# Kernel tuning notes

Hardware: AMD Instinct MI355X
Metric: run time of the kernel (lower is better)

Reference implementation:

```python
import jax, jax.numpy as jnp
import numpy as np
from jax import lax

DIM = 256          # C
D_INNER = 512      # expand * dim
D_STATE = 16       # N
DT_RANK = 32       # ceil(d_inner / 16)
K_CONV = 4


def setup_inputs() -> dict:
    key = jax.random.key(0)
    ks = jax.random.split(key, 20)
    B, C, H, W = 2, DIM, 64, 64
    Di, N, R = D_INNER, D_STATE, DT_RANK
    s = 0.02
    inp = {
        "decoder_feat": jax.random.normal(ks[0], (B, C, H, W), jnp.float32),
        "encoder_feat": jax.random.normal(ks[1], (B, C, H, W), jnp.float32),
        # CrossMambaFusion params
        "dec_w": jax.random.normal(ks[2], (C, 2 * Di), jnp.float32) * s,
        "dec_b": jnp.zeros((2 * Di,), jnp.float32),
        "enc_w": jax.random.normal(ks[3], (C, Di), jnp.float32) * s,
        "enc_b": jnp.zeros((Di,), jnp.float32),
        "out_w": jax.random.normal(ks[4], (Di, C), jnp.float32) * s,
        "out_b": jnp.zeros((C,), jnp.float32),
        "ln_g": jnp.ones((C,), jnp.float32),
        "ln_b": jnp.zeros((C,), jnp.float32),
        # Mamba block params (inner dim = Di, expand=1.0)
        "in_w": jax.random.normal(ks[5], (Di, 2 * Di), jnp.float32) * s,
        "in_b": jnp.zeros((2 * Di,), jnp.float32),
        "conv_w": jax.random.normal(ks[6], (Di, 1, K_CONV), jnp.float32) * 0.1,
        "conv_b": jnp.zeros((Di,), jnp.float32),
        "x_proj_w": jax.random.normal(ks[7], (Di, R + 2 * N), jnp.float32) * s,
        "dt_w": jax.random.normal(ks[8], (R, Di), jnp.float32) * 0.1,
        "dt_b": jax.random.uniform(ks[9], (Di,), jnp.float32, -4.0, -2.0),  # small dt after softplus
        "A_log": jnp.log(jnp.tile(jnp.arange(1, N + 1, dtype=jnp.float32)[None, :], (Di, 1))),
        "D_param": jnp.ones((Di,), jnp.float32),
        "m_out_w": jax.random.normal(ks[10], (Di, Di), jnp.float32) * s,
        "m_out_b": jnp.zeros((Di,), jnp.float32),
    }
    return inp


def _mamba(x, in_w, in_b, conv_w, conv_b, x_proj_w, dt_w, dt_b, A_log, D_param, m_out_w, m_out_b):
    # x: (B, L, Di)
    Bsz, L, Di = x.shape
    N, R = D_STATE, DT_RANK
    xz = x @ in_w + in_b                      # (B, L, 2*Di)
    xm, z = jnp.split(xz, 2, axis=-1)
    # causal depthwise conv over the sequence axis
    xc = jnp.swapaxes(xm, 1, 2)               # (B, Di, L)
    xc = lax.conv_general_dilated(
        xc, conv_w, window_strides=(1,), padding=[(K_CONV - 1, 0)],
        dimension_numbers=("NCH", "OIH", "NCH"), feature_group_count=Di)
    xc = xc + conv_b[None, :, None]
    u = jax.nn.silu(jnp.swapaxes(xc, 1, 2))   # (B, L, Di)
    x_dbl = u @ x_proj_w                      # (B, L, R+2N)
    dt = jax.nn.softplus(x_dbl[..., :R] @ dt_w + dt_b)   # (B, L, Di)
    Bm = x_dbl[..., R:R + N]                  # (B, L, N)
    Cm = x_dbl[..., R + N:]                   # (B, L, N)
    A = -jnp.exp(A_log)                       # (Di, N)

    def step(h, t):
        dt_t, u_t, B_t, C_t = t               # (B,Di),(B,Di),(B,N),(B,N)
        dA = jnp.exp(dt_t[..., None] * A)     # (B, Di, N)
        h = h * dA + (dt_t * u_t)[..., None] * B_t[:, None, :]
        y = jnp.einsum("bdn,bn->bd", h, C_t)
        return h, y

    h0 = jnp.zeros((Bsz, Di, N), x.dtype)
    _, ys = lax.scan(step, h0, (jnp.swapaxes(dt, 0, 1), jnp.swapaxes(u, 0, 1),
                                jnp.swapaxes(Bm, 0, 1), jnp.swapaxes(Cm, 0, 1)))
    y = jnp.swapaxes(ys, 0, 1) + u * D_param  # skip connection via D
    y = y * jax.nn.silu(z)
    return y @ m_out_w + m_out_b


def reference(decoder_feat, encoder_feat, dec_w, dec_b, enc_w, enc_b, out_w, out_b,
              ln_g, ln_b, in_w, in_b, conv_w, conv_b, x_proj_w, dt_w, dt_b,
              A_log, D_param, m_out_w, m_out_b):
    B, C, H, W = decoder_feat.shape
    Di = D_INNER
    dec = jnp.transpose(decoder_feat, (0, 2, 3, 1)).reshape(B, H * W, C)
    enc = jnp.transpose(encoder_feat, (0, 2, 3, 1)).reshape(B, H * W, C)
    dec_proj = dec @ dec_w + dec_b
    dec_x, dec_gate = dec_proj[..., :Di], dec_proj[..., Di:]
    enc_p = enc @ enc_w + enc_b
    combined = dec_x * jax.nn.sigmoid(enc_p) + enc_p          # (B, L, Di)
    processed = _mamba(combined, in_w, in_b, conv_w, conv_b, x_proj_w,
                       dt_w, dt_b, A_log, D_param, m_out_w, m_out_b)
    out = (processed * jax.nn.sigmoid(dec_gate)) @ out_w + out_b
    res = out + dec
    mu = jnp.mean(res, axis=-1, keepdims=True)
    var = jnp.mean(jnp.square(res - mu), axis=-1, keepdims=True)
    res = (res - mu) * lax.rsqrt(var + 1e-5) * ln_g + ln_b
    return jnp.transpose(res.reshape(B, H, W, C), (0, 3, 1, 2))
```

## Files before the change

kernel.cpp:

```cpp
#include <hip/hip_runtime.h>
#include <hip/hip_bf16.h>

typedef __bf16 bf16x8_t __attribute__((ext_vector_type(8)));
typedef float f32x4_t __attribute__((ext_vector_type(4)));

__device__ __forceinline__ float sigmoidf_(float x) { return 1.0f / (1.0f + __expf(-x)); }
__device__ __forceinline__ float siluf_(float x) { return x * sigmoidf_(x); }
__device__ __forceinline__ float softplusf_(float x) {
    return fmaxf(x, 0.0f) + log1pf(__expf(-fabsf(x)));
}
__device__ __forceinline__ float b2f(ushort u) { return __uint_as_float(((unsigned)u) << 16); }
__device__ __forceinline__ ushort f2b(float f) {
    return (ushort)__bfloat16_as_ushort(__float2bfloat16(f));
}

__global__ __launch_bounds__(256) void k_prep(
    const float* __restrict__ dec_w, const float* __restrict__ enc_w,
    const float* __restrict__ in_w, const float* __restrict__ m_out_w,
    const float* __restrict__ out_w, const float* __restrict__ x_proj_w,
    const float* __restrict__ dt_w,
    const float* __restrict__ dec, const float* __restrict__ enc,
    __hip_bfloat16* __restrict__ dec_wT, __hip_bfloat16* __restrict__ enc_wT,
    __hip_bfloat16* __restrict__ in_wT, __hip_bfloat16* __restrict__ m_out_wT,
    __hip_bfloat16* __restrict__ out_wT, __hip_bfloat16* __restrict__ xpwT,
    __hip_bfloat16* __restrict__ dtwT,
    __hip_bfloat16* __restrict__ decL, __hip_bfloat16* __restrict__ encL)
{
    __shared__ float tile[64][65];
    if (blockIdx.x < 5312) {
        int gid = blockIdx.x * 256 + threadIdx.x;
        const float* src; __hip_bfloat16* dst; int lk, N, idx;
        if (gid < 262144)       { src = dec_w;    dst = dec_wT;   lk = 8; N = 1024; idx = gid; }
        else if (gid < 393216)  { src = enc_w;    dst = enc_wT;   lk = 8; N = 512;  idx = gid - 262144; }
        else if (gid < 917504)  { src = in_w;     dst = in_wT;    lk = 9; N = 1024; idx = gid - 393216; }
        else if (gid < 1179648) { src = m_out_w;  dst = m_out_wT; lk = 9; N = 512;  idx = gid - 917504; }
        else if (gid < 1310720) { src = out_w;    dst = out_wT;   lk = 9; N = 256;  idx = gid - 1179648; }
        else if (gid < 1343488) { src = x_proj_w; dst = xpwT;     lk = 9; N = 64;   idx = gid - 1310720; }
        else                    { src = dt_w;     dst = dtwT;     lk = 5; N = 512;  idx = gid - 1343488; }
        int K = 1 << lk;
        int n = idx >> lk, k = idx & (K - 1);
        dst[idx] = __float2bfloat16(src[(size_t)k * N + n]);
        return;
    }
    const int bid = blockIdx.x - 5312;
    const int t = threadIdx.x;
    const int ct = bid & 3;
    const int lt = (bid >> 2) & 63;
    const int sel = bid >> 8;
    const int b = sel & 1, ten = sel >> 1;
    const float* src = ten ? enc : dec;
    __hip_bfloat16* dst = ten ? encL : decL;
    const size_t ibase = (size_t)b * 256 * 4096 + (size_t)(ct * 64) * 4096 + (size_t)lt * 64;
#pragma unroll
    for (int i = 0; i < 16; ++i) {
        int c = i * 4 + (t >> 6), l = t & 63;
        tile[c][l] = src[ibase + (size_t)c * 4096 + l];
    }
    __syncthreads();
    const size_t obase = ((size_t)b * 4096 + (size_t)lt * 64) * 256 + ct * 64;
#pragma unroll
    for (int i = 0; i < 16; ++i) {
        int l = i * 4 + (t >> 6), c = t & 63;
        dst[obase + (size_t)l * 256 + c] = __float2bfloat16(tile[c][l]);
    }
}

template <int EPI, int K>
__global__ __launch_bounds__(256) void bgemm(
    const __hip_bfloat16* __restrict__ A, const __hip_bfloat16* __restrict__ Bt,
    const float* __restrict__ bias, void* __restrict__ out0,
    void* __restrict__ out1, const void* __restrict__ extra)
{
    __shared__ ushort At[128 * 32];
    __shared__ ushort Bl[128 * 32];
    const int tid = threadIdx.x;
    const int wave = tid >> 6, lane = tid & 63;
    const int n0 = blockIdx.x * 128, m0 = blockIdx.y * 128;
    const int wm = (wave >> 1) * 64, wn = (wave & 1) * 64;
    f32x4_t acc[4][4] = {};
    const int fr = lane & 15, fq = (lane >> 4) * 8;

    for (int k0 = 0; k0 < K; k0 += 32) {
#pragma unroll
        for (int q = 0; q < 2; ++q) {
            int idx = q * 256 + tid;
            int row = idx >> 2, ch = (idx & 3) * 8;
            uint4 va = *(const uint4*)&A[(size_t)(m0 + row) * K + k0 + ch];
            uint4 vb = *(const uint4*)&Bt[(size_t)(n0 + row) * K + k0 + ch];
            *(uint4*)&At[row * 32 + ch] = va;
            *(uint4*)&Bl[row * 32 + ch] = vb;
        }
        __syncthreads();
        bf16x8_t af[4], bf[4];
#pragma unroll
        for (int i = 0; i < 4; ++i) {
            af[i] = *(bf16x8_t*)&At[(wm + i * 16 + fr) * 32 + fq];
            bf[i] = *(bf16x8_t*)&Bl[(wn + i * 16 + fr) * 32 + fq];
        }
#pragma unroll
        for (int i = 0; i < 4; ++i)
#pragma unroll
            for (int j = 0; j < 4; ++j)
                acc[i][j] = __builtin_amdgcn_mfma_f32_16x16x32_bf16(af[i], bf[j], acc[i][j], 0, 0, 0);
        __syncthreads();
    }

    const int col = lane & 15, rbase = (lane >> 4) * 4;
#pragma unroll
    for (int i = 0; i < 4; ++i) {
#pragma unroll
        for (int j = 0; j < 4; ++j) {
#pragma unroll
            for (int r = 0; r < 4; ++r) {
                int m = m0 + wm + i * 16 + rbase + r;
                int n = n0 + wn + j * 16 + col;
                float v = acc[i][j][r] + bias[n];
                if (EPI == 0) {
                    ((__hip_bfloat16*)out0)[(size_t)m * 512 + n] = __float2bfloat16(v);
                } else if (EPI == 1) {
                    if (n < 512) {
                        float ep = __bfloat162float(((const __hip_bfloat16*)extra)[(size_t)m * 512 + n]);
                        ((__hip_bfloat16*)out0)[(size_t)m * 512 + n] =
                            __float2bfloat16(fmaf(v, sigmoidf_(ep), ep));
                    } else {
                        ((__hip_bfloat16*)out1)[(size_t)m * 512 + (n - 512)] =
                            __float2bfloat16(sigmoidf_(v));
                    }
                } else if (EPI == 2) {
                    if (n < 512)
                        ((__hip_bfloat16*)out0)[(size_t)m * 512 + n] = __float2bfloat16(v);
                    else
                        ((__hip_bfloat16*)out1)[(size_t)m * 512 + (n - 512)] =
                            __float2bfloat16(siluf_(v));
                } else {
                    float g = __bfloat162float(((const __hip_bfloat16*)extra)[(size_t)m * 512 + n]);
                    ((__hip_bfloat16*)out0)[(size_t)m * 512 + n] = __float2bfloat16(v * g);
                }
            }
        }
    }
}

#define CHUNK 32
#define NCHUNK 128

__global__ __launch_bounds__(512) void k_conv_scan(
    const __hip_bfloat16* __restrict__ xm, const float* __restrict__ conv_w,
    const float* __restrict__ conv_b, const __hip_bfloat16* __restrict__ xpwT,
    const __hip_bfloat16* __restrict__ dtwT, const float* __restrict__ dt_b,
    const float* __restrict__ A_log,
    __hip_bfloat16* __restrict__ u_out, float* __restrict__ Bm,
    float* __restrict__ Cm, __hip_bfloat16* __restrict__ dt_out,
    float* __restrict__ hpart, float* __restrict__ dtsums)
{
    __shared__ __align__(16) ushort us_dts[CHUNK][512 + 8];
    __shared__ __align__(16) ushort adt[CHUNK][32 + 8];
    __shared__ float BsL[CHUNK * 16];
    __shared__ float CsL[CHUNK * 16];
    const int tid = threadIdx.x;
    const int wave = tid >> 6, lane = tid & 63;
    const int bl0 = blockIdx.x * CHUNK;
    const int l0 = bl0 & 4095;
    const int b = blockIdx.x >> 7;
    const int chunk = blockIdx.x & (NCHUNK - 1);
    const int fr = lane & 15, fq = (lane >> 4) * 8;
    const int col = lane & 15, rbase = (lane >> 4) * 4;

    float uarr[CHUNK];
    {
        const int d = tid;
        const float cw0 = conv_w[d * 4], cw1 = conv_w[d * 4 + 1];
        const float cw2 = conv_w[d * 4 + 2], cw3 = conv_w[d * 4 + 3];
        const float cb = conv_b[d];
        const ushort* xs = (const ushort*)xm;
        float x0 = (l0 >= 3) ? b2f(xs[(size_t)(bl0 - 3) * 512 + d]) : 0.f;
        float x1 = (l0 >= 2) ? b2f(xs[(size_t)(bl0 - 2) * 512 + d]) : 0.f;
        float x2 = (l0 >= 1) ? b2f(xs[(size_t)(bl0 - 1) * 512 + d]) : 0.f;
#pragma unroll
        for (int t = 0; t < CHUNK; ++t) {
            float x3 = b2f(xs[(size_t)(bl0 + t) * 512 + d]);
            float a = cb;
            a = fmaf(cw0, x0, a);
            a = fmaf(cw1, x1, a);
            a = fmaf(cw2, x2, a);
            a = fmaf(cw3, x3, a);
            float uv = siluf_(a);
            uarr[t] = uv;
            ushort ub = f2b(uv);
            us_dts[t][d] = ub;
            ((ushort*)u_out)[(size_t)(bl0 + t) * 512 + d] = ub;
            x0 = x1; x1 = x2; x2 = x3;
        }
    }
    __syncthreads();

    {
        const int mi = wave >> 2, n0w = (wave & 3) * 16;
        f32x4_t acc = {};
        const __hip_bfloat16* bp = xpwT + (size_t)(n0w + fr) * 512;
#pragma unroll
        for (int k0 = 0; k0 < 512; k0 += 32) {
            bf16x8_t af = *(bf16x8_t*)&us_dts[mi * 16 + fr][k0 + fq];
            bf16x8_t bf = *(const bf16x8_t*)&bp[k0 + fq];
            acc = __builtin_amdgcn_mfma_f32_16x16x32_bf16(af, bf, acc, 0, 0, 0);
        }
#pragma unroll
        for (int r = 0; r < 4; ++r) {
            int m = mi * 16 + rbase + r;
            int n = n0w + col;
            float v = acc[r];
            if (n < 32) {
                adt[m][n] = f2b(v);
            } else if (n < 48) {
                BsL[m * 16 + (n - 32)] = v;
                Bm[(size_t)(bl0 + m) * 16 + (n - 32)] = v;
            } else {
                CsL[m * 16 + (n - 48)] = v;
                Cm[(size_t)(bl0 + m) * 16 + (n - 48)] = v;
            }
        }
    }
    __syncthreads();

    {
        const int mi = wave >> 2;
        bf16x8_t af = *(bf16x8_t*)&adt[mi * 16 + fr][fq];
#pragma unroll
        for (int t = 0; t < 8; ++t) {
            int nt = (wave & 3) * 8 + t;
            bf16x8_t bf = *(const bf16x8_t*)&dtwT[(size_t)(nt * 16 + fr) * 32 + fq];
            f32x4_t acc = {};
            acc = __builtin_amdgcn_mfma_f32_16x16x32_bf16(af, bf, acc, 0, 0, 0);
#pragma unroll
            for (int r = 0; r < 4; ++r) {
                int m = mi * 16 + rbase + r;
                int n = nt * 16 + col;
                ushort dv = f2b(softplusf_(acc[r] + dt_b[n]));
                us_dts[m][n] = dv;
                ((ushort*)dt_out)[(size_t)(bl0 + m) * 512 + n] = dv;
            }
        }
    }
    __syncthreads();

    {
        const int d = tid;
        float Av[16];
#pragma unroll
        for (int n = 0; n < 16; n += 4) {
            float4 al = *(const float4*)&A_log[d * 16 + n];
            Av[n + 0] = -__expf(al.x);
            Av[n + 1] = -__expf(al.y);
            Av[n + 2] = -__expf(al.z);
            Av[n + 3] = -__expf(al.w);
        }
        float h[16] = {};
        float dtsum = 0.f;
#pragma unroll
        for (int t = 0; t < CHUNK; ++t) {
            float dtv = b2f(us_dts[t][d]);
            float dtu = dtv * uarr[t];
            dtsum += dtv;
            const float* Bt = &BsL[t * 16];
#pragma unroll
            for (int n = 0; n < 16; ++n)
                h[n] = fmaf(h[n], __expf(dtv * Av[n]), dtu * Bt[n]);
        }
        const size_t sidx = ((size_t)b * NCHUNK + chunk) * 512 + d;
        const size_t idx = sidx * 16;
#pragma unroll
        for (int n = 0; n < 16; n += 4)
            *(float4*)&hpart[idx + n] = make_float4(h[n], h[n + 1], h[n + 2], h[n + 3]);
        dtsums[sidx] = dtsum;
    }
}

__global__ __launch_bounds__(256) void k_scan_comb(
    const float* __restrict__ hpart, const float* __restrict__ dtsums,
    const float* __restrict__ A_log, float* __restrict__ h_in)
{
    const int gid = blockIdx.x * 256 + threadIdx.x;
    const int n = gid & 15;
    const int d = (gid >> 4) & 511;
    const int b = gid >> 13;
    const float Av = -__expf(A_log[d * 16 + n]);
    float h = 0.f;
    for (int c = 0; c < NCHUNK; ++c) {
        const size_t sidx = ((size_t)b * NCHUNK + c) * 512 + d;
        const size_t idx = sidx * 16 + n;
        h_in[idx] = h;
        h = fmaf(h, __expf(Av * dtsums[sidx]), hpart[idx]);
    }
}

__global__ __launch_bounds__(512) void k_scan_fin(
    const __hip_bfloat16* __restrict__ dt, const __hip_bfloat16* __restrict__ u,
    const float* __restrict__ Bmp, const float* __restrict__ Cmp,
    const float* __restrict__ A_log, const float* __restrict__ Dp,
    const __hip_bfloat16* __restrict__ zs, const float* __restrict__ h_in,
    __hip_bfloat16* __restrict__ yout)
{
    __shared__ float Bs[CHUNK * 16];
    __shared__ float Cs[CHUNK * 16];
    const int d = threadIdx.x;
    const int chunk = blockIdx.x & (NCHUNK - 1);
    const int b = blockIdx.x >> 7;
    const size_t row0 = (size_t)b * 4096 + (size_t)chunk * CHUNK;

    Bs[d] = Bmp[row0 * 16 + d];
    Cs[d] = Cmp[row0 * 16 + d];
    float Av[16];
#pragma unroll
    for (int n = 0; n < 16; n += 4) {
        float4 al = *(const float4*)&A_log[d * 16 + n];
        Av[n + 0] = -__expf(al.x);
        Av[n + 1] = -__expf(al.y);
        Av[n + 2] = -__expf(al.z);
        Av[n + 3] = -__expf(al.w);
    }
    const float Dv = Dp[d];
    float h[16];
    const size_t idx = (((size_t)b * NCHUNK + chunk) * 512 + d) * 16;
#pragma unroll
    for (int n = 0; n < 16; n += 4) {
        float4 hv = *(const float4*)&h_in[idx + n];
        h[n] = hv.x; h[n + 1] = hv.y; h[n + 2] = hv.z; h[n + 3] = hv.w;
    }
    __syncthreads();

    const ushort* dtp = (const ushort*)dt + row0 * 512 + d;
    const ushort* up = (const ushort*)u + row0 * 512 + d;
    const ushort* zp = (const ushort*)zs + row0 * 512 + d;
    __hip_bfloat16* yp = yout + row0 * 512 + d;
    for (int t = 0; t < CHUNK; ++t) {
        float dtv = b2f(dtp[(size_t)t * 512]);
        float uv = b2f(up[(size_t)t * 512]);
        float zv = b2f(zp[(size_t)t * 512]);
        float dtu = dtv * uv;
        const float* Bt = &Bs[t * 16];
        const float* Ct = &Cs[t * 16];
        float y = 0.f;
#pragma unroll
        for (int n = 0; n < 16; ++n) {
            h[n] = fmaf(h[n], __expf(dtv * Av[n]), dtu * Bt[n]);
            y = fmaf(h[n], Ct[n], y);
        }
        yp[(size_t)t * 512] = __float2bfloat16((y + uv * Dv) * zv);
    }
}

__global__ __launch_bounds__(256) void k_out_ln(
    const __hip_bfloat16* __restrict__ A, const __hip_bfloat16* __restrict__ Bt,
    const float* __restrict__ bias, const __hip_bfloat16* __restrict__ decL,
    const float* __restrict__ ln_g, const float* __restrict__ ln_b,
    float* __restrict__ outp)
{
    __shared__ ushort At[64 * 32];
    __shared__ ushort Bl[256 * 32];
    __shared__ float red[4][64][2];
    __shared__ float lmu[64], lsc[64];
    const int tid = threadIdx.x;
    const int wave = tid >> 6, lane = tid & 63;
    const int m0 = blockIdx.x * 64;
    const int wn = wave * 64;
    f32x4_t acc[4][4] = {};
    const int fr = lane & 15, fq = (lane >> 4) * 8;

    for (int k0 = 0; k0 < 512; k0 += 32) {
        {
            int row = tid >> 2, ch = (tid & 3) * 8;
            *(uint4*)&At[row * 32 + ch] = *(const uint4*)&A[(size_t)(m0 + row) * 512 + k0 + ch];
        }
#pragma unroll
        for (int q = 0; q < 4; ++q) {
            int idx = q * 256 + tid;
            int row = idx >> 2, ch = (idx & 3) * 8;
            *(uint4*)&Bl[row * 32 + ch] = *(const uint4*)&Bt[(size_t)row * 512 + k0 + ch];
        }
        __syncthreads();
        bf16x8_t af[4], bf[4];
#pragma unroll
        for (int i = 0; i < 4; ++i) {
            af[i] = *(bf16x8_t*)&At[(i * 16 + fr) * 32 + fq];
            bf[i] = *(bf16x8_t*)&Bl[(wn + i * 16 + fr) * 32 + fq];
        }
#pragma unroll
        for (int i = 0; i < 4; ++i)
#pragma unroll
            for (int j = 0; j < 4; ++j)
                acc[i][j] = __builtin_amdgcn_mfma_f32_16x16x32_bf16(af[i], bf[j], acc[i][j], 0, 0, 0);
        __syncthreads();
    }

    const int col = lane & 15, rbase = (lane >> 4) * 4;
#pragma unroll
    for (int i = 0; i < 4; ++i) {
#pragma unroll
        for (int r = 0; r < 4; ++r) {
            int ml = i * 16 + rbase + r;
            int m = m0 + ml;
            float s = 0.f, sq = 0.f;
#pragma unroll
            for (int j = 0; j < 4; ++j) {
                int n = wn + j * 16 + col;
                float dv = b2f(((const ushort*)decL)[(size_t)m * 256 + n]);
                float v = acc[i][j][r] + bias[n] + dv;
                acc[i][j][r] = v;
                s += v;
                sq = fmaf(v, v, sq);
            }
            s += __shfl_xor(s, 1);  sq += __shfl_xor(sq, 1);
            s += __shfl_xor(s, 2);  sq += __shfl_xor(sq, 2);
            s += __shfl_xor(s, 4);  sq += __shfl_xor(sq, 4);
            s += __shfl_xor(s, 8);  sq += __shfl_xor(sq, 8);
            if (col == 0) { red[wave][ml][0] = s; red[wave][ml][1] = sq; }
        }
    }
    __syncthreads();
    if (tid < 64) {
        float s  = red[0][tid][0] + red[1][tid][0] + red[2][tid][0] + red[3][tid][0];
        float sq = red[0][tid][1] + red[1][tid][1] + red[2][tid][1] + red[3][tid][1];
        float mu = s * (1.0f / 256.0f);
        float var = sq * (1.0f / 256.0f) - mu * mu;
        lmu[tid] = mu;
        lsc[tid] = rsqrtf(var + 1e-5f);
    }
    __syncthreads();
    const int bb = m0 >> 12;
    const int lpos0 = m0 & 4095;
#pragma unroll
    for (int i = 0; i < 4; ++i) {
#pragma unroll
        for (int r = 0; r < 4; ++r) {
            int ml = i * 16 + rbase + r;
            float mu = lmu[ml], sc = lsc[ml];
#pragma unroll
            for (int j = 0; j < 4; ++j) {
                int n = wn + j * 16 + col;
                float v = (acc[i][j][r] - mu) * sc * ln_g[n] + ln_b[n];
                outp[(size_t)bb * (256 * 4096) + (size_t)n * 4096 + lpos0 + ml] = v;
            }
        }
    }
}

extern "C" void kernel_launch(void* const* d_in, const int* in_sizes, int n_in,
                              void* d_out, int out_size, void* d_ws, size_t ws_size,
                              hipStream_t stream)
{
    const float* decoder_feat = (const float*)d_in[0];
    const float* encoder_feat = (const float*)d_in[1];
    const float* dec_w = (const float*)d_in[2];
    const float* dec_b = (const float*)d_in[3];
    const float* enc_w = (const float*)d_in[4];
    const float* enc_b = (const float*)d_in[5];
    const float* out_w = (const float*)d_in[6];
    const float* out_b = (const float*)d_in[7];
    const float* ln_g = (const float*)d_in[8];
    const float* ln_bb = (const float*)d_in[9];
    const float* in_w = (const float*)d_in[10];
    const float* in_b = (const float*)d_in[11];
    const float* conv_w = (const float*)d_in[12];
    const float* conv_b = (const float*)d_in[13];
    const float* x_proj_w = (const float*)d_in[14];
    const float* dt_w = (const float*)d_in[15];
    const float* dt_b = (const float*)d_in[16];
    const float* A_log = (const float*)d_in[17];
    const float* D_param = (const float*)d_in[18];
    const float* m_out_w = (const float*)d_in[19];
    const float* m_out_b = (const float*)d_in[20];

    float* outp = (float*)d_out;
    char* ws = (char*)d_ws;
    const size_t MB = 1024ull * 1024;
    __hip_bfloat16* decL     = (__hip_bfloat16*)(ws + 0 * MB);
    __hip_bfloat16* encL     = (__hip_bfloat16*)(ws + 4 * MB);
    __hip_bfloat16* dec_wT   = (__hip_bfloat16*)(ws + 8 * MB);
    __hip_bfloat16* enc_wT   = (__hip_bfloat16*)(ws + 9 * MB);
    __hip_bfloat16* in_wT    = (__hip_bfloat16*)(ws + 10 * MB);
    __hip_bfloat16* m_out_wT = (__hip_bfloat16*)(ws + 11 * MB);
    __hip_bfloat16* out_wT   = (__hip_bfloat16*)(ws + 12 * MB);
    __hip_bfloat16* xpwT     = (__hip_bfloat16*)(ws + 12 * MB + 262144);
    __hip_bfloat16* dtwT     = (__hip_bfloat16*)(ws + 12 * MB + 262144 + 65536);
    __hip_bfloat16* enc_pb   = (__hip_bfloat16*)(ws + 13 * MB);
    __hip_bfloat16* combined = (__hip_bfloat16*)(ws + 29 * MB);
    __hip_bfloat16* gate_sig = (__hip_bfloat16*)(ws + 37 * MB);
    __hip_bfloat16* xm       = (__hip_bfloat16*)(ws + 53 * MB);
    __hip_bfloat16* z_silu   = (__hip_bfloat16*)(ws + 61 * MB);
    __hip_bfloat16* u_buf    = (__hip_bfloat16*)(ws + 69 * MB);
    __hip_bfloat16* dt_buf   = (__hip_bfloat16*)(ws + 77 * MB);
    float* Bm                = (float*)(ws + 93 * MB);
    float* Cm                = (float*)(ws + 93 * MB + 524288);
    float* hpart  = (float*)(ws + 13 * MB);
    float* dtsums = (float*)(ws + 21 * MB);
    float* h_in   = (float*)xm;
    __hip_bfloat16* y_buf = combined;
    __hip_bfloat16* gated = xm;

    k_prep<<<6336, 256, 0, stream>>>(
        dec_w, enc_w, in_w, m_out_w, out_w, x_proj_w, dt_w,
        decoder_feat, encoder_feat,
        dec_wT, enc_wT, in_wT, m_out_wT, out_wT, xpwT, dtwT, decL, encL);
    bgemm<0, 256><<<dim3(4, 64), 256, 0, stream>>>(
        encL, enc_wT, enc_b, enc_pb, nullptr, nullptr);
    bgemm<1, 256><<<dim3(8, 64), 256, 0, stream>>>(
        decL, dec_wT, dec_b, combined, gate_sig, enc_pb);
    bgemm<2, 512><<<dim3(8, 64), 256, 0, stream>>>(
        combined, in_wT, in_b, xm, z_silu, nullptr);
    k_conv_scan<<<2 * NCHUNK, 512, 0, stream>>>(
        xm, conv_w, conv_b, xpwT, dtwT, dt_b, A_log,
        u_buf, Bm, Cm, dt_buf, hpart, dtsums);
    k_scan_comb<<<64, 256, 0, stream>>>(hpart, dtsums, A_log, h_in);
    k_scan_fin<<<2 * NCHUNK, 512, 0, stream>>>(
        dt_buf, u_buf, Bm, Cm, A_log, D_param, z_silu, h_in, y_buf);
    bgemm<3, 512><<<dim3(4, 64), 256, 0, stream>>>(
        y_buf, m_out_wT, m_out_b, gated, nullptr, gate_sig);
    k_out_ln<<<128, 256, 0, stream>>>(
        gated, out_wT, out_b, decL, ln_g, ln_bb, outp);
}
```

Baseline: 284.7 us.

## Recompute conv, x_proj and dt in scan-final pass instead of storing intermediates

The conv/scan kernel becomes a template with two modes. The second pass recomputes the causal conv, the x_proj GEMM and the dt projection rather than reading u, dt, B and C from global buffers written by the first pass, and the separate k_scan_fin kernel is removed. This trades about 16MB of intermediate global writes and reads for redundant MFMA and transcendental work in the second pass. Buffer aliasing is changed so h_in and gated get their own workspace regions.

```diff
diff --git a/kernel.cpp b/kernel.cpp
--- a/kernel.cpp
+++ b/kernel.cpp
@@ -144,14 +144,15 @@
 #define CHUNK 32
 #define NCHUNK 128
 
+template <int MODE>
 __global__ __launch_bounds__(512) void k_conv_scan(
     const __hip_bfloat16* __restrict__ xm, const float* __restrict__ conv_w,
     const float* __restrict__ conv_b, const __hip_bfloat16* __restrict__ xpwT,
     const __hip_bfloat16* __restrict__ dtwT, const float* __restrict__ dt_b,
     const float* __restrict__ A_log,
-    __hip_bfloat16* __restrict__ u_out, float* __restrict__ Bm,
-    float* __restrict__ Cm, __hip_bfloat16* __restrict__ dt_out,
-    float* __restrict__ hpart, float* __restrict__ dtsums)
+    float* __restrict__ hpart, float* __restrict__ dtsums,
+    const float* __restrict__ Dp, const __hip_bfloat16* __restrict__ zs,
+    const float* __restrict__ h_in, __hip_bfloat16* __restrict__ yout)
 {
     __shared__ __align__(16) ushort us_dts[CHUNK][512 + 8];
     __shared__ __align__(16) ushort adt[CHUNK][32 + 8];
@@ -186,9 +187,7 @@
             a = fmaf(cw3, x3, a);
             float uv = siluf_(a);
             uarr[t] = uv;
-            ushort ub = f2b(uv);
-            us_dts[t][d] = ub;
-            ((ushort*)u_out)[(size_t)(bl0 + t) * 512 + d] = ub;
+            us_dts[t][d] = f2b(uv);
             x0 = x1; x1 = x2; x2 = x3;
         }
     }
@@ -209,15 +208,9 @@
             int m = mi * 16 + rbase + r;
             int n = n0w + col;
             float v = acc[r];
-            if (n < 32) {
-                adt[m][n] = f2b(v);
-            } else if (n < 48) {
-                BsL[m * 16 + (n - 32)] = v;
-                Bm[(size_t)(bl0 + m) * 16 + (n - 32)] = v;
-            } else {
-                CsL[m * 16 + (n - 48)] = v;
-                Cm[(size_t)(bl0 + m) * 16 + (n - 48)] = v;
-            }
+            if (n < 32)      adt[m][n] = f2b(v);
+            else if (n < 48) BsL[m * 16 + (n - 32)] = v;
+            else             CsL[m * 16 + (n - 48)] = v;
         }
     }
     __syncthreads();
@@ -235,9 +228,7 @@
             for (int r = 0; r < 4; ++r) {
                 int m = mi * 16 + rbase + r;
                 int n = nt * 16 + col;
-                ushort dv = f2b(softplusf_(acc[r] + dt_b[n]));
-                us_dts[m][n] = dv;
-                ((ushort*)dt_out)[(size_t)(bl0 + m) * 512 + n] = dv;
+                us_dts[m][n] = f2b(softplusf_(acc[r] + dt_b[n]));
             }
         }
     }
@@ -254,24 +245,53 @@
             Av[n + 2] = -__expf(al.z);
             Av[n + 3] = -__expf(al.w);
         }
-        float h[16] = {};
-        float dtsum = 0.f;
-#pragma unroll
-        for (int t = 0; t < CHUNK; ++t) {
-            float dtv = b2f(us_dts[t][d]);
-            float dtu = dtv * uarr[t];
-            dtsum += dtv;
-            const float* Bt = &BsL[t * 16];
-#pragma unroll
-            for (int n = 0; n < 16; ++n)
-                h[n] = fmaf(h[n], __expf(dtv * Av[n]), dtu * Bt[n]);
-        }
         const size_t sidx = ((size_t)b * NCHUNK + chunk) * 512 + d;
         const size_t idx = sidx * 16;
-#pragma unroll
-        for (int n = 0; n < 16; n += 4)
-            *(float4*)&hpart[idx + n] = make_float4(h[n], h[n + 1], h[n + 2], h[n + 3]);
-        dtsums[sidx] = dtsum;
+        if (MODE == 0) {
+            float h[16] = {};
+            float dtsum = 0.f;
+#pragma unroll
+            for (int t = 0; t < CHUNK; ++t) {
+                float dtv = b2f(us_dts[t][d]);
+                float dtu = dtv * uarr[t];
+                dtsum += dtv;
+                const float* Bt = &BsL[t * 16];
+#pragma unroll
+                for (int n = 0; n < 16; ++n)
+                    h[n] = fmaf(h[n], __expf(dtv * Av[n]), dtu * Bt[n]);
+            }
+#pragma unroll
+            for (int n = 0; n < 16; n += 4)
+                *(float4*)&hpart[idx + n] = make_float4(h[n], h[n + 1], h[n + 2], h[n + 3]);
+            dtsums[sidx] = dtsum;
+        } else {
+            const float Dv = Dp[d];
+            float h[16];
+#pragma unroll
+            for (int n = 0; n < 16; n += 4) {
+                float4 hv = *(const float4*)&h_in[idx + n];
+                h[n] = hv.x; h[n + 1] = hv.y; h[n + 2] = hv.z; h[n + 3] = hv.w;
+            }
+            const size_t row0 = (size_t)b * 4096 + (size_t)chunk * CHUNK;
+            const ushort* zp = (const ushort*)zs + row0 * 512 + d;
+            ushort* yp = (ushort*)yout + row0 * 512 + d;
+#pragma unroll 4
+            for (int t = 0; t < CHUNK; ++t) {
+                float dtv = b2f(us_dts[t][d]);
+                float uv = uarr[t];
+                float zv = b2f(zp[(size_t)t * 512]);
+                float dtu = dtv * uv;
+                const float* Bt = &BsL[t * 16];
+                const float* Ct = &CsL[t * 16];
+                float y = 0.f;
+#pragma unroll
+                for (int n = 0; n < 16; ++n) {
+                    h[n] = fmaf(h[n], __expf(dtv * Av[n]), dtu * Bt[n]);
+                    y = fmaf(h[n], Ct[n], y);
+                }
+                yp[(size_t)t * 512] = f2b((y + uv * Dv) * zv);
+            }
+        }
     }
 }
 
@@ -290,62 +310,6 @@
         const size_t idx = sidx * 16 + n;
         h_in[idx] = h;
         h = fmaf(h, __expf(Av * dtsums[sidx]), hpart[idx]);
-    }
-}
-
-__global__ __launch_bounds__(512) void k_scan_fin(
-    const __hip_bfloat16* __restrict__ dt, const __hip_bfloat16* __restrict__ u,
-    const float* __restrict__ Bmp, const float* __restrict__ Cmp,
-    const float* __restrict__ A_log, const float* __restrict__ Dp,
-    const __hip_bfloat16* __restrict__ zs, const float* __restrict__ h_in,
-    __hip_bfloat16* __restrict__ yout)
-{
-    __shared__ float Bs[CHUNK * 16];
-    __shared__ float Cs[CHUNK * 16];
-    const int d = threadIdx.x;
-    const int chunk = blockIdx.x & (NCHUNK - 1);
-    const int b = blockIdx.x >> 7;
-    const size_t row0 = (size_t)b * 4096 + (size_t)chunk * CHUNK;
-
-    Bs[d] = Bmp[row0 * 16 + d];
-    Cs[d] = Cmp[row0 * 16 + d];
-    float Av[16];
-#pragma unroll
-    for (int n = 0; n < 16; n += 4) {
-        float4 al = *(const float4*)&A_log[d * 16 + n];
-        Av[n + 0] = -__expf(al.x);
-        Av[n + 1] = -__expf(al.y);
-        Av[n + 2] = -__expf(al.z);
-        Av[n + 3] = -__expf(al.w);
-    }
-    const float Dv = Dp[d];
-    float h[16];
-    const size_t idx = (((size_t)b * NCHUNK + chunk) * 512 + d) * 16;
-#pragma unroll
-    for (int n = 0; n < 16; n += 4) {
-        float4 hv = *(const float4*)&h_in[idx + n];
-        h[n] = hv.x; h[n + 1] = hv.y; h[n + 2] = hv.z; h[n + 3] = hv.w;
-    }
-    __syncthreads();
-
-    const ushort* dtp = (const ushort*)dt + row0 * 512 + d;
-    const ushort* up = (const ushort*)u + row0 * 512 + d;
-    const ushort* zp = (const ushort*)zs + row0 * 512 + d;
-    __hip_bfloat16* yp = yout + row0 * 512 + d;
-    for (int t = 0; t < CHUNK; ++t) {
-        float dtv = b2f(dtp[(size_t)t * 512]);
-        float uv = b2f(up[(size_t)t * 512]);
-        float zv = b2f(zp[(size_t)t * 512]);
-        float dtu = dtv * uv;
-        const float* Bt = &Bs[t * 16];
-        const float* Ct = &Cs[t * 16];
-        float y = 0.f;
-#pragma unroll
-        for (int n = 0; n < 16; ++n) {
-            h[n] = fmaf(h[n], __expf(dtv * Av[n]), dtu * Bt[n]);
-            y = fmaf(h[n], Ct[n], y);
-        }
-        yp[(size_t)t * 512] = __float2bfloat16((y + uv * Dv) * zv);
     }
 }
 
@@ -487,15 +451,11 @@
     __hip_bfloat16* gate_sig = (__hip_bfloat16*)(ws + 37 * MB);
     __hip_bfloat16* xm       = (__hip_bfloat16*)(ws + 53 * MB);
     __hip_bfloat16* z_silu   = (__hip_bfloat16*)(ws + 61 * MB);
-    __hip_bfloat16* u_buf    = (__hip_bfloat16*)(ws + 69 * MB);
-    __hip_bfloat16* dt_buf   = (__hip_bfloat16*)(ws + 77 * MB);
-    float* Bm                = (float*)(ws + 93 * MB);
-    float* Cm                = (float*)(ws + 93 * MB + 524288);
+    __hip_bfloat16* gated    = (__hip_bfloat16*)(ws + 69 * MB);
+    float* h_in              = (float*)(ws + 77 * MB);
     float* hpart  = (float*)(ws + 13 * MB);
     float* dtsums = (float*)(ws + 21 * MB);
-    float* h_in   = (float*)xm;
     __hip_bfloat16* y_buf = combined;
-    __hip_bfloat16* gated = xm;
 
     k_prep<<<6336, 256, 0, stream>>>(
         dec_w, enc_w, in_w, m_out_w, out_w, x_proj_w, dt_w,
@@ -507,12 +467,13 @@
         decL, dec_wT, dec_b, combined, gate_sig, enc_pb);
     bgemm<2, 512><<<dim3(8, 64), 256, 0, stream>>>(
         combined, in_wT, in_b, xm, z_silu, nullptr);
-    k_conv_scan<<<2 * NCHUNK, 512, 0, stream>>>(
+    k_conv_scan<0><<<2 * NCHUNK, 512, 0, stream>>>(
         xm, conv_w, conv_b, xpwT, dtwT, dt_b, A_log,
-        u_buf, Bm, Cm, dt_buf, hpart, dtsums);
+        hpart, dtsums, nullptr, nullptr, nullptr, nullptr);
     k_scan_comb<<<64, 256, 0, stream>>>(hpart, dtsums, A_log, h_in);
-    k_scan_fin<<<2 * NCHUNK, 512, 0, stream>>>(
-        dt_buf, u_buf, Bm, Cm, A_log, D_param, z_silu, h_in, y_buf);
+    k_conv_scan<1><<<2 * NCHUNK, 512, 0, stream>>>(
+        xm, conv_w, conv_b, xpwT, dtwT, dt_b, A_log,
+        nullptr, nullptr, D_param, z_silu, h_in, y_buf);
     bgemm<3, 512><<<dim3(4, 64), 256, 0, stream>>>(
         y_buf, m_out_wT, m_out_b, gated, nullptr, gate_sig);
     k_out_ln<<<128, 256, 0, stream>>>(
```

Measured after the change: 295.9 us. 1.04x slower.
